# Optimization experiments

Hardware: AMD Instinct MI355X
Metric: run time of the kernel (lower is better)

The kernel has to match this reference:

```python
import jax, jax.numpy as jnp
import numpy as np

EPS = 1e-12  # F.normalize eps

def _l2norm(x):
    n = jnp.linalg.norm(x, axis=-1, keepdims=True)
    return x / jnp.maximum(n, EPS)

def setup_inputs() -> dict:
    key = jax.random.key(0)
    ks = jax.random.split(key, 12)
    B, C, D, N, K = 64, 256, 128, 100000, 8
    inp = {
        "query_input": jax.random.normal(ks[0], (B, C), dtype=jnp.float32),
        "keys": jax.random.normal(ks[1], (N, D), dtype=jnp.float32),
        "values": jax.random.normal(ks[2], (N, D), dtype=jnp.float32),
        "importance": jax.random.uniform(ks[3], (N,), dtype=jnp.float32),
        # params (Linear weights stored torch-style: [out, in])
        "W_q": jax.random.normal(ks[4], (D, C), dtype=jnp.float32) / np.sqrt(C),
        "b_q": jax.random.normal(ks[5], (D,), dtype=jnp.float32) * 0.01,
        "w_attn": jax.random.normal(ks[6], (D,), dtype=jnp.float32) / np.sqrt(D),
        "b_attn": jax.random.normal(ks[7], (), dtype=jnp.float32) * 0.01,
        "W_comb": jax.random.normal(ks[8], (D, D), dtype=jnp.float32) / np.sqrt(D),
        "b_comb": jax.random.normal(ks[9], (D,), dtype=jnp.float32) * 0.01,
        "top_k": K,
    }
    return inp

def reference(query_input, keys, values, importance, W_q, b_q, w_attn, b_attn, W_comb, b_comb, top_k):
    # query projection: [B, D]
    q = query_input @ W_q.T + b_q
    # cosine similarity against every bank entry, importance-weighted: [B, N]
    sim = (_l2norm(q) @ _l2norm(keys).T) * importance[None, :]
    # top-k entries per batch row
    _, idx = jax.lax.top_k(sim, top_k)          # [B, K]
    retrieved = values[idx]                      # [B, K, D] gather
    # attention over the K retrieved memories
    scores = jax.nn.softmax(retrieved @ w_attn + b_attn, axis=-1)  # [B, K]
    memory_output = jnp.einsum("bk,bkd->bd", scores, retrieved)
    return memory_output @ W_comb.T + b_comb
```

## Files before the change

kernel.cpp:

```cpp
#include <hip/hip_runtime.h>

typedef __attribute__((ext_vector_type(8))) short short8;
typedef __attribute__((ext_vector_type(4))) float f32x4;

#define BB 64
#define CC 256
#define DD 128
#define NN 100000
#define KK 8

#define CHUNK 128
#define NBLK ((NN + CHUNK - 1) / CHUNK)
#define CPB (NBLK * KK)

__device__ __forceinline__ unsigned short f2bf(float x) {
    unsigned u = __float_as_uint(x);
    unsigned r = u + 0x7fffu + ((u >> 16) & 1u);
    return (unsigned short)(r >> 16);
}

__device__ __forceinline__ void split_bf(float x, unsigned short& h, unsigned short& l) {
    h = f2bf(x);
    float hf = __uint_as_float(((unsigned)h) << 16);
    l = f2bf(x - hf);
}

__device__ __forceinline__ void bfins8(float x, float l[8]) {
#pragma unroll
    for (int s = 0; s < 8; ++s) {
        float hi = fmaxf(l[s], x);
        x = fminf(l[s], x);
        l[s] = hi;
    }
}

__device__ __forceinline__ void bpins8(float v, int ix, float lv[8], int li[8]) {
#pragma unroll
    for (int s = 0; s < 8; ++s) {
        const bool gt = v > lv[s];
        const float nv = gt ? lv[s] : v;
        const int   ni = gt ? li[s] : ix;
        lv[s] = gt ? v : lv[s];
        li[s] = gt ? ix : li[s];
        v = nv; ix = ni;
    }
}

__global__ __launch_bounds__(128) void qproj_kernel(
    const float* __restrict__ query,
    const float* __restrict__ Wq,
    const float* __restrict__ bq,
    unsigned short* __restrict__ qAhi,
    unsigned short* __restrict__ qAlo)
{
    __shared__ float qrow[CC];
    const int tid = threadIdx.x;
    const int b = blockIdx.x;
    for (int i = tid; i < CC; i += 128) qrow[i] = query[b * CC + i];
    __syncthreads();
    float acc = bq[tid];
    const float4* wr = reinterpret_cast<const float4*>(Wq + (size_t)tid * CC);
#pragma unroll 8
    for (int c = 0; c < CC / 4; ++c) {
        float4 w = wr[c];
        acc = fmaf(w.x, qrow[c * 4 + 0], acc);
        acc = fmaf(w.y, qrow[c * 4 + 1], acc);
        acc = fmaf(w.z, qrow[c * 4 + 2], acc);
        acc = fmaf(w.w, qrow[c * 4 + 3], acc);
    }
    unsigned short h, l;
    split_bf(acc, h, l);
    const int d = tid;
    const int mt = b >> 4, n = b & 15;
    const int ks = d >> 5, quad = (d >> 3) & 3, j = d & 7;
    const size_t fi = ((size_t)(mt * 4 + ks) * 64 + quad * 16 + n) * 8 + j;
    qAhi[fi] = h;
    qAlo[fi] = l;
}

__global__ __launch_bounds__(256, 3) void simtopk_kernel(
    const unsigned short* __restrict__ qAhi,
    const unsigned short* __restrict__ qAlo,
    const float* __restrict__ keys,
    const float* __restrict__ imp,
    float* __restrict__ cand_v,
    int* __restrict__ cand_i)
{
    __shared__ float sims[64 * 132];
    __shared__ float c2v[64 * 33];

    const int tid = threadIdx.x;
    const int w = tid >> 6, lane = tid & 63;
    const int p = w >> 1;
    const int h = w & 1;
    const int blk = blockIdx.x;
    const int key0 = blk * CHUNK;
    const int n = lane & 15, quad = lane >> 4;

    short8 Ah[2][4], Al[2][4];
    {
        const short8* GH = reinterpret_cast<const short8*>(qAhi);
        const short8* GL = reinterpret_cast<const short8*>(qAlo);
#pragma unroll
        for (int m2 = 0; m2 < 2; ++m2)
#pragma unroll
            for (int ks = 0; ks < 4; ++ks) {
                const int idx = ((p * 2 + m2) * 4 + ks) * 64 + lane;
                Ah[m2][ks] = GH[idx];
                Al[m2][ks] = GL[idx];
            }
    }

#pragma unroll
    for (int t = 0; t < 4; ++t) {
        const int jl = h * 64 + t * 16 + n;
        const int j = key0 + jl;
        const int jc = (j < NN) ? j : (NN - 1);
        const float* kb = keys + (size_t)jc * DD + quad * 8;

        float4 bv[8];
#pragma unroll
        for (int ks = 0; ks < 4; ++ks) {
            bv[2 * ks]     = *reinterpret_cast<const float4*>(kb + ks * 32);
            bv[2 * ks + 1] = *reinterpret_cast<const float4*>(kb + ks * 32 + 4);
        }

        f32x4 acc[2];
        acc[0] = (f32x4){0.f, 0.f, 0.f, 0.f};
        acc[1] = (f32x4){0.f, 0.f, 0.f, 0.f};
        float ss = 0.f;

#pragma unroll
        for (int ks = 0; ks < 4; ++ks) {
            const float f[8] = {bv[2*ks].x, bv[2*ks].y, bv[2*ks].z, bv[2*ks].w,
                                bv[2*ks+1].x, bv[2*ks+1].y, bv[2*ks+1].z, bv[2*ks+1].w};
            unsigned hw[4], lw[4];
#pragma unroll
            for (int e = 0; e < 4; ++e) {
                const float f0 = f[2 * e], f1 = f[2 * e + 1];
                const unsigned u0 = __float_as_uint(f0), u1 = __float_as_uint(f1);
                hw[e] = __builtin_amdgcn_perm(u1, u0, 0x07060302u);
                const float d0 = f0 - __uint_as_float(u0 & 0xffff0000u);
                const float d1 = f1 - __uint_as_float(u1 & 0xffff0000u);
                lw[e] = __builtin_amdgcn_perm(__float_as_uint(d1), __float_as_uint(d0), 0x07060302u);
                ss = fmaf(f0, f0, fmaf(f1, f1, ss));
            }
            uint4 hv = {hw[0], hw[1], hw[2], hw[3]};
            uint4 lv = {lw[0], lw[1], lw[2], lw[3]};
            short8 Bh = *reinterpret_cast<short8*>(&hv);
            short8 Bl = *reinterpret_cast<short8*>(&lv);
#pragma unroll
            for (int m2 = 0; m2 < 2; ++m2) {
                acc[m2] = __builtin_amdgcn_mfma_f32_16x16x32_bf16(Ah[m2][ks], Bh, acc[m2], 0, 0, 0);
                acc[m2] = __builtin_amdgcn_mfma_f32_16x16x32_bf16(Ah[m2][ks], Bl, acc[m2], 0, 0, 0);
                acc[m2] = __builtin_amdgcn_mfma_f32_16x16x32_bf16(Al[m2][ks], Bh, acc[m2], 0, 0, 0);
            }
        }

        ss += __shfl_xor(ss, 16);
        ss += __shfl_xor(ss, 32);
        const bool valid = (j < NN);
        float scale = 0.f;
        if (valid) scale = imp[j] / fmaxf(sqrtf(ss), 1e-12f);

#pragma unroll
        for (int m2 = 0; m2 < 2; ++m2)
#pragma unroll
            for (int r = 0; r < 4; ++r) {
                const int row = (p * 2 + m2) * 16 + quad * 4 + r;
                const float v = valid ? acc[m2][r] * scale : -1e30f;
                const unsigned packed = (__float_as_uint(v) & ~0x7Fu) | (unsigned)jl;
                sims[row * 132 + jl] = __uint_as_float(packed);
            }
    }
    __syncthreads();

    {
        const int row = tid >> 2, part = tid & 3;
        float v8[8];
#pragma unroll
        for (int s = 0; s < 8; ++s) v8[s] = -1e30f;
        const int base = row * 132 + part * 32;
        const int st = ((row & 15) * 2 + part * 8) & 31;
        for (int i = 0; i < 32; ++i) {
            const int ia = (i + st) & 31;
            bfins8(sims[base + ia], v8);
        }
#pragma unroll
        for (int s = 0; s < 8; ++s) c2v[row * 33 + part * 8 + s] = v8[s];
    }
    __syncthreads();

    if (tid < 64) {
        const int row = tid;
        float v8[8];
#pragma unroll
        for (int s = 0; s < 8; ++s) v8[s] = -1e30f;
        for (int u = 0; u < 32; ++u) bfins8(c2v[row * 33 + u], v8);
        const size_t cbase = (size_t)row * CPB + (size_t)blk * KK;
#pragma unroll
        for (int s = 0; s < 8; ++s) {
            const unsigned bits = __float_as_uint(v8[s]);
            cand_v[cbase + s] = v8[s];
            cand_i[cbase + s] = key0 + (int)(bits & 127u);
        }
    }
}

__global__ __launch_bounds__(256) void mergefinish_kernel(
    const float* __restrict__ cand_v, const int* __restrict__ cand_i,
    const float* __restrict__ values,
    const float* __restrict__ w_attn,
    const float* __restrict__ b_attn,
    const float* __restrict__ W_comb,
    const float* __restrict__ b_comb,
    float* __restrict__ out)
{
    __shared__ float lv[256 * 8];
    __shared__ int   li[256 * 8];
    __shared__ int   tk[KK];
    __shared__ float red[KK][DD];
    __shared__ float tvals[KK];
    __shared__ float mem[DD];

    const int tid = threadIdx.x;
    const int row = blockIdx.x;

    {
        float v8[8]; int i8[8];
#pragma unroll
        for (int s = 0; s < 8; ++s) { v8[s] = -1e30f; i8[s] = 0; }
        const size_t base = (size_t)row * CPB;
        for (int c = tid; c < CPB; c += 256)
            bpins8(cand_v[base + c], cand_i[base + c], v8, i8);
#pragma unroll
        for (int s = 0; s < 8; ++s) { lv[tid * 8 + s] = v8[s]; li[tid * 8 + s] = i8[s]; }
    }
    __syncthreads();

    if (tid < 64) {
        float m8[8]; int mi8[8];
#pragma unroll
        for (int s = 0; s < 8; ++s) { m8[s] = -1e30f; mi8[s] = 0; }
        for (int k2 = 0; k2 < 4; ++k2)
#pragma unroll
            for (int s = 0; s < 8; ++s)
                bpins8(lv[(tid + 64 * k2) * 8 + s], li[(tid + 64 * k2) * 8 + s], m8, mi8);
        for (int rd = 0; rd < KK; ++rd) {
            float m = m8[0];
#pragma unroll
            for (int d = 1; d < 64; d <<= 1) m = fmaxf(m, __shfl_xor(m, d));
            const unsigned long long msk = __ballot(m8[0] == m);
            const int wl = (int)(__ffsll((long long)msk) - 1);
            const int widx = __shfl(mi8[0], wl);
            if (tid == 0) tk[rd] = widx;
            if (tid == wl) {
#pragma unroll
                for (int s = 0; s < 7; ++s) { m8[s] = m8[s + 1]; mi8[s] = mi8[s + 1]; }
                m8[7] = -1e30f;
            }
        }
    }
    __syncthreads();

    float vk[KK];
    if (tid < 128) {
#pragma unroll
        for (int k = 0; k < KK; ++k)
            vk[k] = values[(size_t)tk[k] * DD + tid];
        const float wa = w_attn[tid];
#pragma unroll
        for (int k = 0; k < KK; ++k) red[k][tid] = vk[k] * wa;
    }
    __syncthreads();
    if (tid < KK) {
        float s = 0.f;
        for (int i = 0; i < DD; ++i) s += red[tid][i];
        tvals[tid] = s + b_attn[0];
    }
    __syncthreads();
    if (tid < 128) {
        float m = tvals[0];
#pragma unroll
        for (int k = 1; k < KK; ++k) m = fmaxf(m, tvals[k]);
        float e[KK]; float se = 0.f;
#pragma unroll
        for (int k = 0; k < KK; ++k) { e[k] = expf(tvals[k] - m); se += e[k]; }
        const float inv = 1.f / se;
        float md = 0.f;
#pragma unroll
        for (int k = 0; k < KK; ++k) md += (e[k] * inv) * vk[k];
        mem[tid] = md;
    }
    __syncthreads();
    if (tid < 128) {
        float acc = b_comb[tid];
        const float4* wrow = reinterpret_cast<const float4*>(W_comb + (size_t)tid * DD);
#pragma unroll 8
        for (int c = 0; c < DD / 4; ++c) {
            float4 wv = wrow[c];
            acc = fmaf(wv.x, mem[c * 4 + 0], acc);
            acc = fmaf(wv.y, mem[c * 4 + 1], acc);
            acc = fmaf(wv.z, mem[c * 4 + 2], acc);
            acc = fmaf(wv.w, mem[c * 4 + 3], acc);
        }
        out[row * DD + tid] = acc;
    }
}

extern "C" void kernel_launch(void* const* d_in, const int* in_sizes, int n_in,
                              void* d_out, int out_size, void* d_ws, size_t ws_size,
                              hipStream_t stream) {
    const float* query  = (const float*)d_in[0];
    const float* keys   = (const float*)d_in[1];
    const float* values = (const float*)d_in[2];
    const float* imp    = (const float*)d_in[3];
    const float* Wq     = (const float*)d_in[4];
    const float* bq     = (const float*)d_in[5];
    const float* wattn  = (const float*)d_in[6];
    const float* battn  = (const float*)d_in[7];
    const float* Wcomb  = (const float*)d_in[8];
    const float* bcomb  = (const float*)d_in[9];

    unsigned short* qAhi = (unsigned short*)d_ws;
    unsigned short* qAlo = qAhi + 8192;
    float* cand_v = (float*)(qAlo + 8192);
    int*   cand_i = (int*)(cand_v + (size_t)BB * CPB);

    qproj_kernel<<<BB, 128, 0, stream>>>(query, Wq, bq, qAhi, qAlo);
    simtopk_kernel<<<NBLK, 256, 0, stream>>>(qAhi, qAlo, keys, imp, cand_v, cand_i);
    mergefinish_kernel<<<BB, 256, 0, stream>>>(cand_v, cand_i, values, wattn, battn,
                                               Wcomb, bcomb, (float*)d_out);
}
```

Before: 171.0 us.

## Drop candidate index array, rebuild key index from packed bits and slot

The similarity kernel no longer writes a separate candidate index array. The key's low 7 bits are already packed into the float value, so the merge kernel reconstructs the global key index from the candidate slot's chunk number plus those bits. Candidate values are written and read as float4, the second-stage scratch array is removed by reusing the sims shared buffer (adding an extra barrier), and the occupancy hint rises to 4 blocks per CU. This halves candidate traffic and shared memory use, but the reconstruction has to match the slot layout exactly.

```diff
diff --git a/kernel.cpp b/kernel.cpp
--- a/kernel.cpp
+++ b/kernel.cpp
@@ -78,16 +78,14 @@
     qAlo[fi] = l;
 }
 
-__global__ __launch_bounds__(256, 3) void simtopk_kernel(
+__global__ __launch_bounds__(256, 4) void simtopk_kernel(
     const unsigned short* __restrict__ qAhi,
     const unsigned short* __restrict__ qAlo,
     const float* __restrict__ keys,
     const float* __restrict__ imp,
-    float* __restrict__ cand_v,
-    int* __restrict__ cand_i)
+    float* __restrict__ cand_v)
 {
     __shared__ float sims[64 * 132];
-    __shared__ float c2v[64 * 33];
 
     const int tid = threadIdx.x;
     const int w = tid >> 6, lane = tid & 63;
@@ -175,40 +173,44 @@
     }
     __syncthreads();
 
+    float v8[8];
     {
         const int row = tid >> 2, part = tid & 3;
-        float v8[8];
 #pragma unroll
         for (int s = 0; s < 8; ++s) v8[s] = -1e30f;
         const int base = row * 132 + part * 32;
-        const int st = ((row & 15) * 2 + part * 8) & 31;
+        const int st = ((row & 15) + part * 8) & 31;
         for (int i = 0; i < 32; ++i) {
             const int ia = (i + st) & 31;
             bfins8(sims[base + ia], v8);
         }
-#pragma unroll
-        for (int s = 0; s < 8; ++s) c2v[row * 33 + part * 8 + s] = v8[s];
+    }
+    __syncthreads();
+
+    {
+        const int row = tid >> 2, part = tid & 3;
+        float4* dst = reinterpret_cast<float4*>(&sims[row * 132 + part * 8]);
+        dst[0] = (float4){v8[0], v8[1], v8[2], v8[3]};
+        dst[1] = (float4){v8[4], v8[5], v8[6], v8[7]};
     }
     __syncthreads();
 
     if (tid < 64) {
         const int row = tid;
-        float v8[8];
-#pragma unroll
-        for (int s = 0; s < 8; ++s) v8[s] = -1e30f;
-        for (int u = 0; u < 32; ++u) bfins8(c2v[row * 33 + u], v8);
-        const size_t cbase = (size_t)row * CPB + (size_t)blk * KK;
-#pragma unroll
-        for (int s = 0; s < 8; ++s) {
-            const unsigned bits = __float_as_uint(v8[s]);
-            cand_v[cbase + s] = v8[s];
-            cand_i[cbase + s] = key0 + (int)(bits & 127u);
-        }
+        float m8[8];
+#pragma unroll
+        for (int s = 0; s < 8; ++s) m8[s] = -1e30f;
+        const int st = (3 * row) & 31;
+        for (int u = 0; u < 32; ++u)
+            bfins8(sims[row * 132 + ((u + st) & 31)], m8);
+        float4* out4 = reinterpret_cast<float4*>(cand_v + (size_t)row * CPB + (size_t)blk * KK);
+        out4[0] = (float4){m8[0], m8[1], m8[2], m8[3]};
+        out4[1] = (float4){m8[4], m8[5], m8[6], m8[7]};
     }
 }
 
 __global__ __launch_bounds__(256) void mergefinish_kernel(
-    const float* __restrict__ cand_v, const int* __restrict__ cand_i,
+    const float* __restrict__ cand_v,
     const float* __restrict__ values,
     const float* __restrict__ w_attn,
     const float* __restrict__ b_attn,
@@ -230,9 +232,15 @@
         float v8[8]; int i8[8];
 #pragma unroll
         for (int s = 0; s < 8; ++s) { v8[s] = -1e30f; i8[s] = 0; }
-        const size_t base = (size_t)row * CPB;
-        for (int c = tid; c < CPB; c += 256)
-            bpins8(cand_v[base + c], cand_i[base + c], v8, i8);
+        const float4* cv4 = reinterpret_cast<const float4*>(cand_v + (size_t)row * CPB);
+        for (int c4 = tid; c4 < CPB / 4; c4 += 256) {
+            const float4 v = cv4[c4];
+            const int c = c4 * 4;
+            bpins8(v.x, c + 0, v8, i8);
+            bpins8(v.y, c + 1, v8, i8);
+            bpins8(v.z, c + 2, v8, i8);
+            bpins8(v.w, c + 3, v8, i8);
+        }
 #pragma unroll
         for (int s = 0; s < 8; ++s) { lv[tid * 8 + s] = v8[s]; li[tid * 8 + s] = i8[s]; }
     }
@@ -252,8 +260,9 @@
             for (int d = 1; d < 64; d <<= 1) m = fmaxf(m, __shfl_xor(m, d));
             const unsigned long long msk = __ballot(m8[0] == m);
             const int wl = (int)(__ffsll((long long)msk) - 1);
-            const int widx = __shfl(mi8[0], wl);
-            if (tid == 0) tk[rd] = widx;
+            const int wc = __shfl(mi8[0], wl);
+            if (tid == 0)
+                tk[rd] = (wc >> 3) * CHUNK + (int)(__float_as_uint(m) & 127u);
             if (tid == wl) {
 #pragma unroll
                 for (int s = 0; s < 7; ++s) { m8[s] = m8[s + 1]; mi8[s] = mi8[s + 1]; }
@@ -325,10 +334,9 @@
     unsigned short* qAhi = (unsigned short*)d_ws;
     unsigned short* qAlo = qAhi + 8192;
     float* cand_v = (float*)(qAlo + 8192);
-    int*   cand_i = (int*)(cand_v + (size_t)BB * CPB);
 
     qproj_kernel<<<BB, 128, 0, stream>>>(query, Wq, bq, qAhi, qAlo);
-    simtopk_kernel<<<NBLK, 256, 0, stream>>>(qAhi, qAlo, keys, imp, cand_v, cand_i);
-    mergefinish_kernel<<<BB, 256, 0, stream>>>(cand_v, cand_i, values, wattn, battn,
+    simtopk_kernel<<<NBLK, 256, 0, stream>>>(qAhi, qAlo, keys, imp, cand_v);
+    mergefinish_kernel<<<BB, 256, 0, stream>>>(cand_v, values, wattn, battn,
                                                Wcomb, bcomb, (float*)d_out);
 }
```

Result: faster. 163.1 us (-4.7%).
